# Optimization experiments

Measured on AMD Instinct MI355X. Metric: run time of the kernel, lower is better.

Reference implementation:

```python
import jax, jax.numpy as jnp
import numpy as np

DECAY = 0.99
EPS = 1e-05
N, K, D = 32768, 8192, 64


def setup_inputs() -> dict:
    key = jax.random.key(0)
    k1, k2, k3 = jax.random.split(key, 3)
    return {
        "inputs": jax.random.normal(k1, (N, D), dtype=jnp.float32),
        "embedding_w": jax.random.normal(k2, (K, D), dtype=jnp.float32),
        "ema_w": jax.random.normal(k3, (K, D), dtype=jnp.float32),
        "ema_cluster_size": jnp.zeros((K,), dtype=jnp.float32),
    }


def reference(inputs, embedding_w, ema_w, ema_cluster_size):
    k = embedding_w.shape[0]
    # pairwise squared L2 distances: [N, K]
    distances = (
        jnp.sum(inputs ** 2, axis=1, keepdims=True)
        + jnp.sum(embedding_w ** 2, axis=1)
        - 2.0 * inputs @ embedding_w.T
    )
    encoding_indices = jnp.argmin(distances, axis=1)           # [N] int
    encodings = jax.nn.one_hot(encoding_indices, k, dtype=inputs.dtype)  # [N, K]
    codebook = embedding_w  # returned codebook is the PRE-update weight (as in torch source)

    # EMA updates (training branch), expressed functionally
    cluster_size = ema_cluster_size * DECAY + (1.0 - DECAY) * jnp.sum(encodings, axis=0)
    n = jnp.sum(cluster_size)
    cluster_size = (cluster_size + EPS) / (n + k * EPS) * n
    dw = encodings.T @ inputs                                   # [K, D]
    ema_w_new = ema_w * DECAY + (1.0 - DECAY) * dw
    embedding_new = ema_w_new / cluster_size[:, None]

    return (encodings, codebook, cluster_size, ema_w_new, embedding_new)
```

## Files before the change

kernel.cpp:

```cpp
#include <hip/hip_runtime.h>
#include <hip/hip_bf16.h>

#define N_PTS 32768
#define K_CLU 8192
#define D_DIM 64
#define DECAYF 0.99f
#define OMDF   0.01f
#define EPSF   1e-5f

typedef _Float16 v8h __attribute__((ext_vector_type(8)));
typedef float    v4f __attribute__((ext_vector_type(4)));

#define AS1 __attribute__((address_space(1)))
#define AS3 __attribute__((address_space(3)))

#define OFF_COUNTS 0
#define OFF_DW     (32768)
#define OFF_NSUM   (OFF_DW + 2097152)
#define OFF_EHI    (OFF_NSUM + 16)
#define OFF_ELO    (OFF_EHI + 1048576)
#define OFF_E2     (OFF_ELO + 1048576)

__global__ __launch_bounds__(256) void vq_prep(
    const float* __restrict__ emb, const float* __restrict__ ema_cs,
    _Float16* __restrict__ ehi, _Float16* __restrict__ elo,
    float* __restrict__ e2, float* __restrict__ nsum)
{
    const int wave = threadIdx.x >> 6;
    const int lane = threadIdx.x & 63;
    if (blockIdx.x < 2048) {
        const int row = blockIdx.x * 4 + wave;
        float v = emb[(size_t)row * D_DIM + lane];
        _Float16 h = (_Float16)v;
        _Float16 l = (_Float16)(v - (float)h);
        const int sw = (lane & 7) | ((((lane >> 3) ^ (row & 7)) & 7) << 3);
        ehi[(size_t)row * D_DIM + sw] = h;
        elo[(size_t)row * D_DIM + sw] = l;
        float s = v * v;
        #pragma unroll
        for (int m = 1; m < 64; m <<= 1) s += __shfl_xor(s, m, 64);
        if (lane == 0) e2[row] = s;
    } else {
        const int t = (blockIdx.x - 2048) * 256 + threadIdx.x;
        float v = ema_cs[t];
        #pragma unroll
        for (int m = 1; m < 64; m <<= 1) v += __shfl_xor(v, m, 64);
        if (lane == 0) atomicAdd(nsum, v);
    }
}

__global__ __launch_bounds__(256, 4) void vq_fused(
    const float* __restrict__ x,
    const _Float16* __restrict__ ehi, const _Float16* __restrict__ elo,
    const float* __restrict__ e2,
    float* __restrict__ enc,
    unsigned int* __restrict__ counts,
    float* __restrict__ dw)
{
    __shared__ _Float16 sEhi[2][64 * 64];
    __shared__ _Float16 sElo[2][64 * 64];
    __shared__ float    sE2[2][64];

    const int bid  = blockIdx.x;
    const int tid  = threadIdx.x;
    const int wave = tid >> 6;
    const int lane = tid & 63;
    const int quad = lane >> 4;
    const int l15  = lane & 15;
    const int ptbase = bid * 64 + wave * 16;

    v8h xh[2], xl[2];
    {
        const int pt = ptbase + l15;
        const float* xp = x + (size_t)pt * D_DIM + quad * 8;
        #pragma unroll
        for (int c = 0; c < 2; ++c) {
            float4 a = *(const float4*)(xp + c * 32);
            float4 b = *(const float4*)(xp + c * 32 + 4);
            float vv[8] = {a.x, a.y, a.z, a.w, b.x, b.y, b.z, b.w};
            v8h hh, ll;
            #pragma unroll
            for (int j = 0; j < 8; ++j) {
                _Float16 h = (_Float16)vv[j];
                hh[j] = h;
                ll[j] = (_Float16)(vv[j] - (float)h);
            }
            xh[c] = hh; xl[c] = ll;
        }
    }

    float best[4]; int bidx4[4];
    #pragma unroll
    for (int i = 0; i < 4; ++i) { best[i] = 3.4e38f; bidx4[i] = 0; }

    v4f* enc4 = (v4f*)enc;
    const size_t zbase = (size_t)bid * 131072 + tid;
    const v4f zz = {0.f, 0.f, 0.f, 0.f};

    auto stage = [&](int b, int chunk) {
        const size_t gb = (size_t)chunk * 64 * 128;
        const char* gh = (const char*)ehi + gb;
        const char* gl = (const char*)elo + gb;
        char* lh = (char*)&sEhi[b][0];
        char* ll = (char*)&sElo[b][0];
        #pragma unroll
        for (int i = 0; i < 2; ++i) {
            const int off = wave * 2048 + i * 1024;
            __builtin_amdgcn_global_load_lds(
                (const AS1 void*)(gh + off + lane * 16), (AS3 void*)(lh + off), 16, 0, 0);
            __builtin_amdgcn_global_load_lds(
                (const AS1 void*)(gl + off + lane * 16), (AS3 void*)(ll + off), 16, 0, 0);
        }
        if (wave == 0) {
            const char* ge = (const char*)(e2 + (size_t)chunk * 64);
            char* le = (char*)&sE2[b][0];
            __builtin_amdgcn_global_load_lds(
                (const AS1 void*)(ge + lane * 4), (AS3 void*)le, 4, 0, 0);
        }
    };

    stage(0, 0);
    __syncthreads();

    for (int chunk = 0; chunk < 128; ++chunk) {
        const int cur = chunk & 1;
        if (chunk + 1 < 128) stage(cur ^ 1, chunk + 1);

        const int kbase = chunk * 64;
        const size_t zo = zbase + (size_t)chunk * 1024;
        #pragma unroll
        for (int sub = 0; sub < 4; ++sub) {
            __builtin_nontemporal_store(zz, enc4 + zo + sub * 256);

            const int nl = sub * 16 + l15;
            const int ro = nl * 64;
            const int swz = (nl & 7) << 3;
            v8h bh0 = *(const v8h*)&sEhi[cur][ro + ((quad << 3) ^ swz)];
            v8h bh1 = *(const v8h*)&sEhi[cur][ro + (((4 + quad) << 3) ^ swz)];
            v8h bl0 = *(const v8h*)&sElo[cur][ro + ((quad << 3) ^ swz)];
            v8h bl1 = *(const v8h*)&sElo[cur][ro + (((4 + quad) << 3) ^ swz)];
            const float e2v = sE2[cur][nl];
            const int kidx = kbase + nl;
            v4f acc0 = {0.f, 0.f, 0.f, 0.f};
            v4f acc1 = {0.f, 0.f, 0.f, 0.f};
            acc0 = __builtin_amdgcn_mfma_f32_16x16x32_f16(xh[0], bh0, acc0, 0, 0, 0);
            acc1 = __builtin_amdgcn_mfma_f32_16x16x32_f16(xh[1], bh1, acc1, 0, 0, 0);
            acc0 = __builtin_amdgcn_mfma_f32_16x16x32_f16(xl[0], bh0, acc0, 0, 0, 0);
            acc1 = __builtin_amdgcn_mfma_f32_16x16x32_f16(xl[1], bh1, acc1, 0, 0, 0);
            acc0 = __builtin_amdgcn_mfma_f32_16x16x32_f16(xh[0], bl0, acc0, 0, 0, 0);
            acc1 = __builtin_amdgcn_mfma_f32_16x16x32_f16(xh[1], bl1, acc1, 0, 0, 0);
            #pragma unroll
            for (int r = 0; r < 4; ++r) {
                float dot = acc0[r] + acc1[r];
                float dist = fmaf(dot, -2.0f, e2v);
                if (dist < best[r]) { best[r] = dist; bidx4[r] = kidx; }
            }
        }
        __syncthreads();
    }

    #pragma unroll
    for (int i = 0; i < 4; ++i) {
        #pragma unroll
        for (int m = 1; m < 16; m <<= 1) {
            float ov = __shfl_xor(best[i], m, 64);
            int   oi = __shfl_xor(bidx4[i], m, 64);
            if (ov < best[i] || (ov == best[i] && oi < bidx4[i])) { best[i] = ov; bidx4[i] = oi; }
        }
    }

    __syncthreads();

    if (l15 == 0) {
        #pragma unroll
        for (int r = 0; r < 4; ++r) {
            int p = ptbase + quad * 4 + r;
            enc[(size_t)p * K_CLU + bidx4[r]] = 1.0f;
            atomicAdd(&counts[bidx4[r]], 1u);
        }
    }

    #pragma unroll
    for (int j = 0; j < 16; ++j) {
        const int src = (j >> 2) * 16;
        const int r = j & 3;
        int k = __shfl(bidx4[r], src, 64);
        float val = x[(size_t)(ptbase + j) * D_DIM + lane];
        atomicAdd(&dw[(size_t)k * D_DIM + lane], val);
    }
}

__global__ __launch_bounds__(256) void vq_finalize(
    const float* __restrict__ emb, const float* __restrict__ ema_w,
    const float* __restrict__ ema_cs,
    const unsigned int* __restrict__ counts, const float* __restrict__ dw,
    const float* __restrict__ nsum,
    float* __restrict__ out)
{
    const size_t ENC = (size_t)N_PTS * K_CLU;
    float* out_codebook = out + ENC;
    float* out_cs       = out_codebook + (size_t)K_CLU * D_DIM;
    float* out_ema      = out_cs + K_CLU;
    float* out_emb      = out_ema + (size_t)K_CLU * D_DIM;

    const int gid = blockIdx.x * 256 + threadIdx.x;
    const int k = gid >> 6, d = gid & 63;
    float dwv = dw[gid];
    float en  = DECAYF * ema_w[gid] + OMDF * dwv;
    float cnt = (float)counts[k];
    float cs_raw = DECAYF * ema_cs[k] + OMDF * cnt;
    float n  = DECAYF * nsum[0] + OMDF * (float)N_PTS;
    float cs = (cs_raw + EPSF) / (n + (float)K_CLU * EPSF) * n;
    out_codebook[gid] = emb[gid];
    out_ema[gid] = en;
    out_emb[gid] = en / cs;
    if (d == 0) out_cs[k] = cs;
}

extern "C" void kernel_launch(void* const* d_in, const int* in_sizes, int n_in,
                              void* d_out, int out_size, void* d_ws, size_t ws_size,
                              hipStream_t stream)
{
    const float* x      = (const float*)d_in[0];
    const float* emb    = (const float*)d_in[1];
    const float* ema_w  = (const float*)d_in[2];
    const float* ema_cs = (const float*)d_in[3];
    float* out = (float*)d_out;
    char* ws = (char*)d_ws;

    unsigned int* counts = (unsigned int*)(ws + OFF_COUNTS);
    float*        dw     = (float*)(ws + OFF_DW);
    float*        nsum   = (float*)(ws + OFF_NSUM);
    _Float16*     ehi    = (_Float16*)(ws + OFF_EHI);
    _Float16*     elo    = (_Float16*)(ws + OFF_ELO);
    float*        e2     = (float*)(ws + OFF_E2);

    hipMemsetAsync(ws + OFF_COUNTS, 0, (OFF_NSUM + 16) - OFF_COUNTS, stream);

    vq_prep<<<2080, 256, 0, stream>>>(emb, ema_cs, ehi, elo, e2, nsum);
    vq_fused<<<512, 256, 0, stream>>>(x, ehi, elo, e2, out, counts, dw);
    vq_finalize<<<2048, 256, 0, stream>>>(emb, ema_w, ema_cs, counts, dw, nsum, out);
}
```

Before: 1.074 ms.

## Pre-tile codebook into MFMA fragment layout and read operands directly from global

The prep kernel now writes the fp16 hi/lo codebook in a layout where each 16-row group is already arranged as the per-lane MFMA B-fragment. The main kernel drops LDS double-buffering, async global-to-LDS staging and per-chunk barriers, and each wave loads its B fragments straight from global/L2 with unroll 4. The aim is to remove barrier stalls and LDS traffic. In exchange every wave re-reads the whole codebook from cache with no sharing inside the block, so L2 bandwidth and latency hiding now rest on occupancy and unrolling. The launch-bounds occupancy hint is also removed.

```diff
diff --git a/kernel.cpp b/kernel.cpp
--- a/kernel.cpp
+++ b/kernel.cpp
@@ -10,9 +10,6 @@
 
 typedef _Float16 v8h __attribute__((ext_vector_type(8)));
 typedef float    v4f __attribute__((ext_vector_type(4)));
-
-#define AS1 __attribute__((address_space(1)))
-#define AS3 __attribute__((address_space(3)))
 
 #define OFF_COUNTS 0
 #define OFF_DW     (32768)
@@ -33,9 +30,11 @@
         float v = emb[(size_t)row * D_DIM + lane];
         _Float16 h = (_Float16)v;
         _Float16 l = (_Float16)(v - (float)h);
-        const int sw = (lane & 7) | ((((lane >> 3) ^ (row & 7)) & 7) << 3);
-        ehi[(size_t)row * D_DIM + sw] = h;
-        elo[(size_t)row * D_DIM + sw] = l;
+        const int g = row >> 4, r = row & 15;
+        const int c = lane >> 5, q = (lane >> 3) & 3, j = lane & 7;
+        const int idx = g * 1024 + c * 512 + q * 128 + r * 8 + j;
+        ehi[idx] = h;
+        elo[idx] = l;
         float s = v * v;
         #pragma unroll
         for (int m = 1; m < 64; m <<= 1) s += __shfl_xor(s, m, 64);
@@ -49,7 +48,7 @@
     }
 }
 
-__global__ __launch_bounds__(256, 4) void vq_fused(
+__global__ __launch_bounds__(256) void vq_fused(
     const float* __restrict__ x,
     const _Float16* __restrict__ ehi, const _Float16* __restrict__ elo,
     const float* __restrict__ e2,
@@ -57,10 +56,6 @@
     unsigned int* __restrict__ counts,
     float* __restrict__ dw)
 {
-    __shared__ _Float16 sEhi[2][64 * 64];
-    __shared__ _Float16 sElo[2][64 * 64];
-    __shared__ float    sE2[2][64];
-
     const int bid  = blockIdx.x;
     const int tid  = threadIdx.x;
     const int wave = tid >> 6;
@@ -97,66 +92,32 @@
     const size_t zbase = (size_t)bid * 131072 + tid;
     const v4f zz = {0.f, 0.f, 0.f, 0.f};
 
-    auto stage = [&](int b, int chunk) {
-        const size_t gb = (size_t)chunk * 64 * 128;
-        const char* gh = (const char*)ehi + gb;
-        const char* gl = (const char*)elo + gb;
-        char* lh = (char*)&sEhi[b][0];
-        char* ll = (char*)&sElo[b][0];
-        #pragma unroll
-        for (int i = 0; i < 2; ++i) {
-            const int off = wave * 2048 + i * 1024;
-            __builtin_amdgcn_global_load_lds(
-                (const AS1 void*)(gh + off + lane * 16), (AS3 void*)(lh + off), 16, 0, 0);
-            __builtin_amdgcn_global_load_lds(
-                (const AS1 void*)(gl + off + lane * 16), (AS3 void*)(ll + off), 16, 0, 0);
-        }
-        if (wave == 0) {
-            const char* ge = (const char*)(e2 + (size_t)chunk * 64);
-            char* le = (char*)&sE2[b][0];
-            __builtin_amdgcn_global_load_lds(
-                (const AS1 void*)(ge + lane * 4), (AS3 void*)le, 4, 0, 0);
-        }
-    };
-
-    stage(0, 0);
-    __syncthreads();
-
-    for (int chunk = 0; chunk < 128; ++chunk) {
-        const int cur = chunk & 1;
-        if (chunk + 1 < 128) stage(cur ^ 1, chunk + 1);
-
-        const int kbase = chunk * 64;
-        const size_t zo = zbase + (size_t)chunk * 1024;
-        #pragma unroll
-        for (int sub = 0; sub < 4; ++sub) {
-            __builtin_nontemporal_store(zz, enc4 + zo + sub * 256);
-
-            const int nl = sub * 16 + l15;
-            const int ro = nl * 64;
-            const int swz = (nl & 7) << 3;
-            v8h bh0 = *(const v8h*)&sEhi[cur][ro + ((quad << 3) ^ swz)];
-            v8h bh1 = *(const v8h*)&sEhi[cur][ro + (((4 + quad) << 3) ^ swz)];
-            v8h bl0 = *(const v8h*)&sElo[cur][ro + ((quad << 3) ^ swz)];
-            v8h bl1 = *(const v8h*)&sElo[cur][ro + (((4 + quad) << 3) ^ swz)];
-            const float e2v = sE2[cur][nl];
-            const int kidx = kbase + nl;
-            v4f acc0 = {0.f, 0.f, 0.f, 0.f};
-            v4f acc1 = {0.f, 0.f, 0.f, 0.f};
-            acc0 = __builtin_amdgcn_mfma_f32_16x16x32_f16(xh[0], bh0, acc0, 0, 0, 0);
-            acc1 = __builtin_amdgcn_mfma_f32_16x16x32_f16(xh[1], bh1, acc1, 0, 0, 0);
-            acc0 = __builtin_amdgcn_mfma_f32_16x16x32_f16(xl[0], bh0, acc0, 0, 0, 0);
-            acc1 = __builtin_amdgcn_mfma_f32_16x16x32_f16(xl[1], bh1, acc1, 0, 0, 0);
-            acc0 = __builtin_amdgcn_mfma_f32_16x16x32_f16(xh[0], bl0, acc0, 0, 0, 0);
-            acc1 = __builtin_amdgcn_mfma_f32_16x16x32_f16(xh[1], bl1, acc1, 0, 0, 0);
-            #pragma unroll
-            for (int r = 0; r < 4; ++r) {
-                float dot = acc0[r] + acc1[r];
-                float dist = fmaf(dot, -2.0f, e2v);
-                if (dist < best[r]) { best[r] = dist; bidx4[r] = kidx; }
-            }
-        }
-        __syncthreads();
+    #pragma unroll 4
+    for (int g = 0; g < 512; ++g) {
+        __builtin_nontemporal_store(zz, enc4 + zbase + (size_t)g * 256);
+
+        const _Float16* bh = ehi + g * 1024;
+        const _Float16* bl = elo + g * 1024;
+        v8h bh0 = ((const v8h*)(bh      ))[lane];
+        v8h bh1 = ((const v8h*)(bh + 512))[lane];
+        v8h bl0 = ((const v8h*)(bl      ))[lane];
+        v8h bl1 = ((const v8h*)(bl + 512))[lane];
+        const float e2v = e2[g * 16 + l15];
+        const int kidx = g * 16 + l15;
+        v4f acc0 = {0.f, 0.f, 0.f, 0.f};
+        v4f acc1 = {0.f, 0.f, 0.f, 0.f};
+        acc0 = __builtin_amdgcn_mfma_f32_16x16x32_f16(xh[0], bh0, acc0, 0, 0, 0);
+        acc1 = __builtin_amdgcn_mfma_f32_16x16x32_f16(xh[1], bh1, acc1, 0, 0, 0);
+        acc0 = __builtin_amdgcn_mfma_f32_16x16x32_f16(xl[0], bh0, acc0, 0, 0, 0);
+        acc1 = __builtin_amdgcn_mfma_f32_16x16x32_f16(xl[1], bh1, acc1, 0, 0, 0);
+        acc0 = __builtin_amdgcn_mfma_f32_16x16x32_f16(xh[0], bl0, acc0, 0, 0, 0);
+        acc1 = __builtin_amdgcn_mfma_f32_16x16x32_f16(xh[1], bl1, acc1, 0, 0, 0);
+        #pragma unroll
+        for (int r = 0; r < 4; ++r) {
+            float dot = acc0[r] + acc1[r];
+            float dist = fmaf(dot, -2.0f, e2v);
+            if (dist < best[r]) { best[r] = dist; bidx4[r] = kidx; }
+        }
     }
 
     #pragma unroll
```

Result: no change. 1.095 ms (+2.0%).
